# Performance work log

Measured on AMD Instinct MI355X. Metric: run time of the kernel, lower is better.

## Reference

```python
import jax, jax.numpy as jnp
import numpy as np

ALPHA = 0.4
MAX_STEPS = 10
GATE_WARMUP = 1.0

def _l2n(x):  # F.normalize(dim=-1), eps=1e-12
    return x / jnp.maximum(jnp.linalg.norm(x, axis=-1, keepdims=True), 1e-12)

def _ln(x, g, b):  # nn.LayerNorm, eps=1e-5
    m = jnp.mean(x, -1, keepdims=True)
    v = jnp.mean((x - m) ** 2, -1, keepdims=True)
    return (x - m) * jax.lax.rsqrt(v + 1e-5) * g + b

def _gelu(x):  # torch F.gelu default = exact erf
    return jax.nn.gelu(x, approximate=False)

def setup_inputs() -> dict:
    key = jax.random.key(0)
    ks = jax.random.split(key, 12)
    B, T, V, D, H = 4, 256, 50257, 768, 3072
    f32 = jnp.float32
    s = lambda k, shape, sc: jax.random.normal(k, shape, dtype=f32) * sc
    return {
        'token_ids': jax.random.randint(ks[0], (B, T), 0, V),
        'embedding': s(ks[1], (V, D), 0.02),      # nn.Embedding table
        'V0': s(ks[2], (D, H), 0.02), 'b0': jnp.zeros((H,), f32),  # hierarchy layer 0
        'V1': s(ks[3], (H, D), 0.02), 'b1': jnp.zeros((D,), f32),  # hierarchy layer 1
        'W1': s(ks[4], (D, D), 0.005), 'c1': jnp.zeros((D,), f32), # core_proj[0]
        'W2': s(ks[5], (D, D), 0.005), 'c2': jnp.zeros((D,), f32), # core_proj[2]
        'Wg': s(ks[6], (2 * D, D), 0.005), 'bg': jnp.zeros((D,), f32),  # gate_proj
        'Wt': s(ks[7], (D, D), 0.01),              # temporal_proj (no bias)
        'gamma': jnp.ones((D,), f32), 'beta': jnp.zeros((D,), f32),    # out_norm
        'Wl': s(ks[8], (D, V), 0.02),              # lm_head (no bias)
        'R_weight': s(ks[9], (D, D), 0.01),        # buffer (orthogonal-ish, small)
    }

def reference(token_ids, embedding, V0, b0, V1, b1, W1, c1, W2, c2, Wg, bg, Wt, gamma, beta, Wl, R_weight):
    B = token_ids.shape[0]
    D = embedding.shape[1]

    def step(carry, idx):
        h_prev, x2 = carry  # h_prev: [B,D] recurrent state; x2: settled hierarchy state [B,D]
        emb = _l2n(embedding[idx])                       # [B,D]
        h_prev_d = jax.lax.stop_gradient(h_prev)         # .detach()
        temporal_raw = h_prev_d @ R_weight               # [B,D]
        ctx = emb + ALPHA * temporal_raw
        # hierarchy.infer_and_learn under no_grad: iterative relaxation toward the
        # feedforward settled state over max_steps iterations.
        ctx_d = jax.lax.stop_gradient(ctx)
        target = _gelu(_gelu(ctx_d @ V0 + b0) @ V1 + b1)
        x2 = jax.lax.fori_loop(0, MAX_STEPS, lambda i, x: 0.5 * x + 0.5 * target, x2)
        x2 = jax.lax.stop_gradient(x2)
        core_settled = _l2n(x2)
        # differentiable shadow path through V0/b0/V1/b1
        core_shadow = _l2n(_gelu(_gelu(ctx @ V0 + b0) @ V1 + b1))
        core_blended = 0.5 * core_shadow + 0.5 * core_settled
        core_feat = _gelu(core_blended @ W1 + c1) @ W2 + c2      # core_proj MLP
        temporal_feat = temporal_raw @ Wt
        gate = jax.nn.sigmoid(jnp.concatenate([emb, core_feat], axis=-1) @ Wg + bg)
        g = gate * GATE_WARMUP
        h_t = g * (core_feat + ALPHA * temporal_feat) + (1.0 - g) * emb
        h_t = _ln(h_t, gamma, beta)
        logits = h_t @ Wl                                # [B,V]
        return (jax.lax.stop_gradient(h_t), x2), logits

    init = (jnp.zeros((B, D), embedding.dtype), jnp.zeros((B, D), embedding.dtype))
    _, logits = jax.lax.scan(step, init, token_ids.T)    # [T,B,V]
    return jnp.transpose(logits, (1, 0, 2))              # [B,T,V]
```

## Files before the change

### kernel.cpp

```cpp
#include <hip/hip_runtime.h>


typedef __attribute__((ext_vector_type(8))) short short8;
typedef __attribute__((ext_vector_type(4))) float f32x4;
typedef unsigned long long u64;

__device__ __forceinline__ unsigned short f2b(float f){
  unsigned int u = __builtin_bit_cast(unsigned int, f);
  u += 0x7fffu + ((u >> 16) & 1u);
  return (unsigned short)(u >> 16);
}
__device__ __forceinline__ float b2f(unsigned short v){
  return __builtin_bit_cast(float, ((unsigned int)v) << 16);
}
__device__ __forceinline__ float geluf(float x){
  return 0.5f * x * (1.0f + erff(x * 0.70710678118654752440f));
}
__device__ __forceinline__ float wsum(float v){
  #pragma unroll
  for (int o = 32; o; o >>= 1) v += __shfl_xor(v, o, 64);
  return v;
}
__device__ __forceinline__ u64 pk3t(float a, float b, float c, unsigned tag){
  return (u64)f2b(a) | ((u64)f2b(b) << 16) | ((u64)f2b(c) << 32) | ((u64)(tag & 0xffffu) << 48);
}
__device__ __forceinline__ void st64(u64* p, u64 v){
  __hip_atomic_store(p, v, __ATOMIC_RELAXED, __HIP_MEMORY_SCOPE_AGENT);
}
__device__ __forceinline__ void stflag(int* p, int v){
  __hip_atomic_store(p, v, __ATOMIC_RELAXED, __HIP_MEMORY_SCOPE_AGENT);
}
__device__ __forceinline__ int ldflag(const int* p){
  return __hip_atomic_load(p, __ATOMIC_RELAXED, __HIP_MEMORY_SCOPE_AGENT);
}
__device__ __forceinline__ void vm0(){ asm volatile("s_waitcnt vmcnt(0)" ::: "memory"); }

#define FA1  0
#define FTG  256
#define FU   512
#define FPRE 768
#define F2A1  1024
#define F2TG  1088
#define F2U   1152
#define F2PRE 1216

__global__ __launch_bounds__(256) void transpose_f2b(
    const float* __restrict__ src, unsigned short* __restrict__ dst,
    int N, int rowoff)
{
  __shared__ unsigned short tile[32][33];
  const int nb = blockIdx.x * 32, kb = blockIdx.y * 32;
  const int tx = threadIdx.x & 31, ty = threadIdx.x >> 5;
  #pragma unroll
  for (int i = 0; i < 4; ++i) {
    int k = kb + ty + 8*i, n = nb + tx;
    unsigned short v = 0;
    if (n < N) v = f2b(src[(size_t)(rowoff + k)*N + n]);
    tile[ty + 8*i][tx] = v;
  }
  __syncthreads();
  #pragma unroll
  for (int i = 0; i < 4; ++i) {
    int n = nb + ty + 8*i;
    if (n < N) dst[(size_t)n*768 + kb + tx] = tile[tx][ty + 8*i];
  }
}

__global__ __launch_bounds__(256) void embed_kernel(
    const int* __restrict__ tok, const float* __restrict__ emb,
    float* __restrict__ emb_all)
{
  const int row = blockIdx.x, tid = threadIdx.x;
  const int id = tok[row];
  const float* e = emb + (size_t)id * 768;
  float v0 = e[tid], v1 = e[tid+256], v2 = e[tid+512];
  float ssq = wsum(v0*v0 + v1*v1 + v2*v2);
  __shared__ float red[4];
  if ((tid & 63) == 0) red[tid >> 6] = ssq;
  __syncthreads();
  float inv = 1.0f / fmaxf(sqrtf(red[0]+red[1]+red[2]+red[3]), 1e-12f);
  float* o = emb_all + (size_t)row * 768;
  o[tid] = v0*inv; o[tid+256] = v1*inv; o[tid+512] = v2*inv;
}

__global__ void gbias_kernel(const float* __restrict__ c2,
                             const float* __restrict__ Wg,
                             float* __restrict__ gbias)
{
  int c = blockIdx.x * 256 + threadIdx.x;
  if (c >= 768) return;
  float s = 0.f;
  for (int k = 0; k < 768; ++k) s += c2[k] * Wg[(size_t)(768 + k)*768 + c];
  gbias[c] = s;
}

template<int BMODE>
__global__ __launch_bounds__(256) void gemm_kernel(
    const float* __restrict__ A, const void* __restrict__ Bp,
    float* __restrict__ C, const float* __restrict__ bias,
    int M, int N, int q, int r)
{
  const int x = blockIdx.x;
  const int s = blockIdx.y;
  const int mtiles = M >> 6;
  const int cnt_x = q + (x < r ? 1 : 0);
  if (s >= cnt_x * mtiles) return;
  const int off_x = x*q + (x < r ? x : r);
  const int nt = off_x + s / mtiles;
  const int mt = s % mtiles;
  const int m0 = mt << 6, n0 = nt << 6;
  const int w = threadIdx.x >> 6, l = threadIdx.x & 63;
  const int lrow = l & 15, lk8 = (l >> 4) << 3;
  const int arow = m0 + w*16 + lrow;
  f32x4 acc[4] = {f32x4{0,0,0,0}, f32x4{0,0,0,0}, f32x4{0,0,0,0}, f32x4{0,0,0,0}};
  const unsigned short* BT = (const unsigned short*)Bp;
  const float* Bf = (const float*)Bp;

  for (int kk = 0; kk < 768; kk += 32) {
    const float4* ap = (const float4*)(A + (size_t)arow*768 + kk + lk8);
    float4 a0 = ap[0], a1 = ap[1];
    short8 af;
    af[0]=(short)f2b(a0.x); af[1]=(short)f2b(a0.y); af[2]=(short)f2b(a0.z); af[3]=(short)f2b(a0.w);
    af[4]=(short)f2b(a1.x); af[5]=(short)f2b(a1.y); af[6]=(short)f2b(a1.z); af[7]=(short)f2b(a1.w);
    #pragma unroll
    for (int ss = 0; ss < 4; ++ss) {
      const int col = n0 + ss*16 + lrow;
      short8 bf;
      if (BMODE == 0) {
        if (col < N) {
          uint4 raw = *(const uint4*)(BT + (size_t)col*768 + kk + lk8);
          bf = __builtin_bit_cast(short8, raw);
        } else {
          bf = short8{0,0,0,0,0,0,0,0};
        }
      } else {
        #pragma unroll
        for (int j = 0; j < 8; ++j) {
          float v = (col < N) ? Bf[(size_t)(kk + lk8 + j)*N + col] : 0.f;
          bf[j] = (short)f2b(v);
        }
      }
      acc[ss] = __builtin_amdgcn_mfma_f32_16x16x32_bf16(af, bf, acc[ss], 0, 0, 0);
    }
  }
  const int rbase = m0 + w*16 + ((l >> 4) << 2);
  #pragma unroll
  for (int ss = 0; ss < 4; ++ss) {
    const int col = n0 + ss*16 + lrow;
    if (col < N) {
      const float badd = bias ? bias[col] : 0.f;
      #pragma unroll
      for (int rr = 0; rr < 4; ++rr)
        C[(size_t)(rbase + rr)*N + col] = acc[ss][rr] + badd;
    }
  }
}

__global__ __launch_bounds__(256) void recur_kernel(
    const float* __restrict__ RV0, const float* __restrict__ RWt,
    const float* __restrict__ W1,  const float* __restrict__ W2,
    const float* __restrict__ W2G, const float* __restrict__ V1,
    const float* __restrict__ embV0, const float* __restrict__ embWg,
    const float* __restrict__ gbias, const float* __restrict__ emb_all,
    const float* __restrict__ b1, const float* __restrict__ c1,
    const float* __restrict__ c2, const float* __restrict__ gam,
    const float* __restrict__ bet, float* __restrict__ h_all,
    u64* __restrict__ a1_if, u64* __restrict__ tg_if,
    u64* __restrict__ u_if,  u64* __restrict__ pre_if,
    int* __restrict__ flg)
{
  __shared__ float sRV0[12*768];
  __shared__ float sV1[3*3072];
  __shared__ float sW1[3*768];
  __shared__ float sW2[3*768];
  __shared__ float sW2G[3*768];
  __shared__ float sRWt[3*768];
  __shared__ float sX[4*768];
  __shared__ float sX2[4*768];
  __shared__ unsigned short sA1[4*3072];
  __shared__ float sRed[240];
  __shared__ float sTf[16];

  const int g = blockIdx.x, tid = threadIdx.x;
  const int wv = tid >> 6, lane = tid & 63;
  const bool isAgg = (g < 16);

  for (int i = tid; i < 12*768; i += 256) {
    int k = i / 12, c = i - k*12;
    sRV0[c*768 + k] = RV0[(size_t)k*3072 + g*12 + c];
  }
  for (int i = tid; i < 3*3072; i += 256) {
    int k = i / 3, c = i - k*3;
    sV1[c*3072 + k] = V1[(size_t)k*768 + g*3 + c];
  }
  for (int i = tid; i < 3*768; i += 256) {
    int k = i / 3, c = i - k*3;
    const int gc = g*3 + c;
    sW1[c*768 + k]  = W1[(size_t)k*768 + gc];
    sW2[c*768 + k]  = W2[(size_t)k*768 + gc];
    sW2G[c*768 + k] = W2G[(size_t)k*768 + gc];
    sRWt[c*768 + k] = RWt[(size_t)k*768 + gc];
  }
  for (int i = tid; i < 4*768; i += 256) sX2[i] = 0.f;
  __syncthreads();

  for (int t = 0; t <= 256; ++t) {
    if (t == 0) {
      for (int i = tid; i < 4*768; i += 256) sX[i] = 0.f;
    } else {
      if (isAgg) {
        if (tid < 16)
          while (ldflag(flg + FPRE + g*16 + tid) < t) __builtin_amdgcn_s_sleep(2);
        __syncthreads();
        if (tid == 0) stflag(flg + F2PRE + g, t);
      }
      if (tid < 16)
        while (ldflag(flg + F2PRE + tid) < t) __builtin_amdgcn_s_sleep(4);
      __syncthreads();
      const u64* pm = pre_if + (size_t)(t-1)*1024 + lane*16 + wv;
      u64 w4[4];
      #pragma unroll
      for (int qq = 0; qq < 4; ++qq) w4[qq] = pm[qq*4];
      float pre[12];
      #pragma unroll
      for (int qq = 0; qq < 4; ++qq) {
        pre[qq*3+0] = b2f((unsigned short)(w4[qq]));
        pre[qq*3+1] = b2f((unsigned short)(w4[qq] >> 16));
        pre[qq*3+2] = b2f((unsigned short)(w4[qq] >> 32));
      }
      float s1 = 0.f;
      #pragma unroll
      for (int i = 0; i < 12; ++i) s1 += pre[i];
      s1 = wsum(s1);
      const float mean = s1 * (1.0f/768.0f);
      float s2 = 0.f;
      #pragma unroll
      for (int i = 0; i < 12; ++i) { const float d = pre[i] - mean; s2 += d*d; }
      s2 = wsum(s2);
      const float rstd = 1.0f / sqrtf(s2*(1.0f/768.0f) + 1e-5f);
      const int k0 = lane*12;
      float hv[12];
      #pragma unroll
      for (int i = 0; i < 12; ++i) {
        hv[i] = (pre[i] - mean)*rstd*gam[k0+i] + bet[k0+i];
        sX[wv*768 + k0 + i] = hv[i];
      }
      if (g == 0) {
        float* hp = h_all + (size_t)(wv*256 + t - 1)*768 + k0;
        #pragma unroll
        for (int i = 0; i < 12; ++i) hp[i] = hv[i];
      }
    }
    __syncthreads();
    if (t == 256) break;
    const unsigned tagp = (unsigned)(t + 1);
    const int want = t + 1;

    {
      const int cg = tid >> 6, ks = tid & 63;
      float acc[4][4] = {};
      for (int i = 0; i < 12; ++i) {
        const int k = ks + 64*i;
        const float x0 = sX[k], x1 = sX[768+k], x2v = sX[1536+k], x3 = sX[2304+k];
        #pragma unroll
        for (int j = 0; j < 4; ++j) {
          float w;
          if (cg < 3) w = sRV0[(cg*4 + j)*768 + k];
          else        w = (j < 3) ? sRWt[j*768 + k] : 0.f;
          acc[j][0] += w*x0; acc[j][1] += w*x1; acc[j][2] += w*x2v; acc[j][3] += w*x3;
        }
      }
      #pragma unroll
      for (int j = 0; j < 4; ++j)
        #pragma unroll
        for (int bb = 0; bb < 4; ++bb) {
          const float v = wsum(acc[j][bb]);
          if (lane == 0) sRed[cg*16 + j*4 + bb] = v;
        }
      __syncthreads();
      if (tid < 16) {
        const int bb = tid & 3, w = tid >> 2;
        float v[3];
        #pragma unroll
        for (int s = 0; s < 3; ++s) {
          const int c = w*3 + s;
          const float raw = sRed[(c >> 2)*16 + (c & 3)*4 + bb];
          v[s] = geluf(embV0[(size_t)(bb*256 + t)*3072 + g*12 + c] + 0.4f*raw);
        }
        st64(a1_if + (size_t)t*4096 + bb*1024 + g*4 + w, pk3t(v[0], v[1], v[2], tagp));
      } else if (tid < 20) {
        const int bb = tid - 16;
        sTf[bb]     = sRed[48 + bb];
        sTf[4 + bb] = sRed[52 + bb];
        sTf[8 + bb] = sRed[56 + bb];
      }
      vm0();
      __syncthreads();
      if (tid == 0) stflag(flg + FA1 + g, want);
    }

    {
      if (isAgg) {
        if (tid < 16)
          while (ldflag(flg + FA1 + g*16 + tid) < want) __builtin_amdgcn_s_sleep(2);
        __syncthreads();
        if (tid == 0) stflag(flg + F2A1 + g, want);
      }
      if (tid < 16)
        while (ldflag(flg + F2A1 + tid) < want) __builtin_amdgcn_s_sleep(4);
      __syncthreads();
      const u64* basep = a1_if + (size_t)t*4096;
      u64 x[16];
      #pragma unroll
      for (int i = 0; i < 16; ++i) x[i] = basep[i*256 + tid];
      #pragma unroll
      for (int i = 0; i < 16; ++i) {
        const int widx = i*256 + tid;
        const int bb = widx >> 10, j = widx & 1023;
        sA1[bb*3072 + 3*j + 0] = (unsigned short)(x[i]);
        sA1[bb*3072 + 3*j + 1] = (unsigned short)(x[i] >> 16);
        sA1[bb*3072 + 3*j + 2] = (unsigned short)(x[i] >> 32);
      }
      __syncthreads();
      const int ks = lane, isub = wv;
      float acc[3][4] = {};
      for (int ip = 0; ip < 12; ++ip) {
        const int k = ks + 64*(isub + 4*ip);
        float xv[4];
        #pragma unroll
        for (int bb = 0; bb < 4; ++bb) xv[bb] = b2f(sA1[bb*3072 + k]);
        #pragma unroll
        for (int c = 0; c < 3; ++c) {
          const float w = sV1[c*3072 + k];
          acc[c][0] += w*xv[0]; acc[c][1] += w*xv[1]; acc[c][2] += w*xv[2]; acc[c][3] += w*xv[3];
        }
      }
      #pragma unroll
      for (int c = 0; c < 3; ++c)
        #pragma unroll
        for (int bb = 0; bb < 4; ++bb) {
          const float v = wsum(acc[c][bb]);
          if (lane == 0) sRed[isub*12 + c*4 + bb] = v;
        }
      __syncthreads();
      if (tid < 4) {
        const int bb = tid;
        float v[3];
        #pragma unroll
        for (int c = 0; c < 3; ++c) {
          float s = sRed[c*4+bb] + sRed[12 + c*4+bb] + sRed[24 + c*4+bb] + sRed[36 + c*4+bb];
          v[c] = geluf(s + b1[g*3 + c]);
        }
        st64(tg_if + (size_t)t*1024 + g*4 + bb, pk3t(v[0], v[1], v[2], tagp));
      }
      vm0();
      __syncthreads();
      if (tid == 0) stflag(flg + FTG + g, want);
    }

    {
      if (isAgg) {
        if (tid < 16)
          while (ldflag(flg + FTG + g*16 + tid) < want) __builtin_amdgcn_s_sleep(2);
        __syncthreads();
        if (tid == 0) stflag(flg + F2TG + g, want);
      }
      if (tid < 16)
        while (ldflag(flg + F2TG + tid) < want) __builtin_amdgcn_s_sleep(4);
      __syncthreads();
      const u64* pm = tg_if + (size_t)t*1024 + lane*16 + wv;
      u64 w4[4];
      #pragma unroll
      for (int qq = 0; qq < 4; ++qq) w4[qq] = pm[qq*4];
      float tv[12];
      #pragma unroll
      for (int qq = 0; qq < 4; ++qq) {
        tv[qq*3+0] = b2f((unsigned short)(w4[qq]));
        tv[qq*3+1] = b2f((unsigned short)(w4[qq] >> 16));
        tv[qq*3+2] = b2f((unsigned short)(w4[qq] >> 32));
      }
      const int xb = wv*768 + lane*12;
      float xv2[12];
      float ssqT = 0.f, ssqX = 0.f;
      #pragma unroll
      for (int i = 0; i < 12; ++i) {
        float xx = sX2[xb + i];
        const float tt = tv[i];
        #pragma unroll
        for (int rr = 0; rr < 10; ++rr) xx = 0.5f*xx + 0.5f*tt;
        sX2[xb + i] = xx; xv2[i] = xx;
        ssqT += tt*tt; ssqX += xx*xx;
      }
      ssqT = wsum(ssqT); ssqX = wsum(ssqX);
      const float invT = 1.0f / fmaxf(sqrtf(ssqT), 1e-12f);
      const float invX = 1.0f / fmaxf(sqrtf(ssqX), 1e-12f);
      #pragma unroll
      for (int i = 0; i < 12; ++i) sX[xb + i] = 0.5f*(tv[i]*invT + xv2[i]*invX);
      __syncthreads();
      const int ks = lane, isub = wv;
      float acc[3][4] = {};
      #pragma unroll
      for (int ip = 0; ip < 3; ++ip) {
        const int k = ks + 64*(isub + 4*ip);
        float xv[4];
        #pragma unroll
        for (int bb = 0; bb < 4; ++bb) xv[bb] = sX[bb*768 + k];
        #pragma unroll
        for (int c = 0; c < 3; ++c) {
          const float w = sW1[c*768 + k];
          acc[c][0] += w*xv[0]; acc[c][1] += w*xv[1]; acc[c][2] += w*xv[2]; acc[c][3] += w*xv[3];
        }
      }
      #pragma unroll
      for (int c = 0; c < 3; ++c)
        #pragma unroll
        for (int bb = 0; bb < 4; ++bb) {
          const float v = wsum(acc[c][bb]);
          if (lane == 0) sRed[isub*12 + c*4 + bb] = v;
        }
      __syncthreads();
      if (tid < 4) {
        const int bb = tid;
        float v[3];
        #pragma unroll
        for (int c = 0; c < 3; ++c) {
          float s = sRed[c*4+bb] + sRed[12 + c*4+bb] + sRed[24 + c*4+bb] + sRed[36 + c*4+bb];
          v[c] = geluf(s + c1[g*3 + c]);
        }
        st64(u_if + (size_t)t*1024 + g*4 + bb, pk3t(v[0], v[1], v[2], tagp));
      }
      vm0();
      __syncthreads();
      if (tid == 0) stflag(flg + FU + g, want);
    }

    {
      if (isAgg) {
        if (tid < 16)
          while (ldflag(flg + FU + g*16 + tid) < want) __builtin_amdgcn_s_sleep(2);
        __syncthreads();
        if (tid == 0) stflag(flg + F2U + g, want);
      }
      if (tid < 16)
        while (ldflag(flg + F2U + tid) < want) __builtin_amdgcn_s_sleep(4);
      __syncthreads();
      const u64* pm = u_if + (size_t)t*1024 + lane*16 + wv;
      u64 w4[4];
      #pragma unroll
      for (int qq = 0; qq < 4; ++qq) w4[qq] = pm[qq*4];
      const int xb = wv*768 + lane*12;
      #pragma unroll
      for (int qq = 0; qq < 4; ++qq) {
        sX[xb + qq*3 + 0] = b2f((unsigned short)(w4[qq]));
        sX[xb + qq*3 + 1] = b2f((unsigned short)(w4[qq] >> 16));
        sX[xb + qq*3 + 2] = b2f((unsigned short)(w4[qq] >> 32));
      }
      __syncthreads();
      const int ks = lane, isub = wv;
      float acc[6][4] = {};
      #pragma unroll
      for (int ip = 0; ip < 3; ++ip) {
        const int k = ks + 64*(isub + 4*ip);
        float xv[4];
        #pragma unroll
        for (int bb = 0; bb < 4; ++bb) xv[bb] = sX[bb*768 + k];
        #pragma unroll
        for (int c = 0; c < 6; ++c) {
          const float w = (c < 3) ? sW2[c*768 + k] : sW2G[(c-3)*768 + k];
          acc[c][0] += w*xv[0]; acc[c][1] += w*xv[1]; acc[c][2] += w*xv[2]; acc[c][3] += w*xv[3];
        }
      }
      #pragma unroll
      for (int c = 0; c < 6; ++c)
        #pragma unroll
        for (int bb = 0; bb < 4; ++bb) {
          const float v = wsum(acc[c][bb]);
          if (lane == 0) sRed[isub*24 + c*4 + bb] = v;
        }
      __syncthreads();
      if (tid < 4) {
        const int bb = tid;
        float pre3[3];
        #pragma unroll
        for (int c = 0; c < 3; ++c) {
          const int col = g*3 + c;
          float sc = sRed[c*4+bb] + sRed[24 + c*4+bb] + sRed[48 + c*4+bb] + sRed[72 + c*4+bb];
          const float cf = sc + c2[col];
          const int cc = c + 3;
          float sg = sRed[cc*4+bb] + sRed[24 + cc*4+bb] + sRed[48 + cc*4+bb] + sRed[72 + cc*4+bb];
          const float gv = sg + embWg[(size_t)(bb*256 + t)*768 + col] + gbias[col];
          const float gg = 1.0f / (1.0f + expf(-gv));
          const float em = emb_all[(size_t)(bb*256 + t)*768 + col];
          pre3[c] = gg*(cf + 0.4f*sTf[c*4 + bb]) + (1.0f - gg)*em;
        }
        st64(pre_if + (size_t)t*1024 + g*4 + bb, pk3t(pre3[0], pre3[1], pre3[2], tagp));
      }
      vm0();
      __syncthreads();
      if (tid == 0) stflag(flg + FPRE + g, want);
    }
  }
}

static void launch_gemm(const float* A, const void* B, float* C, const float* bias,
                        int M, int N, int bmode, hipStream_t st)
{
  const int ntiles = (N + 63) / 64;
  const int q = ntiles / 8, r = ntiles % 8;
  const int mtiles = M / 64;
  const int smax = (q + (r ? 1 : 0)) * mtiles;
  dim3 grid(8, smax);
  if (bmode == 0) gemm_kernel<0><<<grid, 256, 0, st>>>(A, B, C, bias, M, N, q, r);
  else            gemm_kernel<1><<<grid, 256, 0, st>>>(A, B, C, bias, M, N, q, r);
}

extern "C" void kernel_launch(void* const* d_in, const int* in_sizes, int n_in,
                              void* d_out, int out_size, void* d_ws, size_t ws_size,
                              hipStream_t stream)
{
  const int*   tok   = (const int*)d_in[0];
  const float* emb   = (const float*)d_in[1];
  const float* V0    = (const float*)d_in[2];
  const float* b0    = (const float*)d_in[3];
  const float* V1    = (const float*)d_in[4];
  const float* b1    = (const float*)d_in[5];
  const float* W1    = (const float*)d_in[6];
  const float* c1    = (const float*)d_in[7];
  const float* W2    = (const float*)d_in[8];
  const float* c2    = (const float*)d_in[9];
  const float* Wg    = (const float*)d_in[10];
  const float* bg    = (const float*)d_in[11];
  const float* Wt    = (const float*)d_in[12];
  const float* gamma = (const float*)d_in[13];
  const float* beta  = (const float*)d_in[14];
  const float* Wl    = (const float*)d_in[15];
  const float* Rw    = (const float*)d_in[16];

  float* outf = (float*)d_out;
  float* emb_all = outf + 0;
  float* RV0     = outf + 786432;
  float* RWt     = outf + 3145728;
  float* W2G     = outf + 3735552;
  float* embV0   = outf + 4325376;
  float* embWg   = outf + 7471104;
  float* gbias   = outf + 8257536;
  unsigned short* V0T  = (unsigned short*)(outf + 8258560);
  unsigned short* WtT  = (unsigned short*)(outf + 9438208);
  unsigned short* WgTT = (unsigned short*)(outf + 9733120);
  unsigned short* WgBT = (unsigned short*)(outf + 10028032);
  u64* a1_if  = (u64*)(outf + 10322944);
  u64* tg_if  = (u64*)(outf + 12428288);
  u64* u_if   = (u64*)(outf + 12954624);
  u64* pre_if = (u64*)(outf + 13480960);
  int* flg    = (int*)(outf + 14007296);

  float* h_all = (float*)d_ws;
  unsigned short* WlT = (unsigned short*)((char*)d_ws + 786432*4);
  const bool bigws = ws_size >= (size_t)(786432*4) + (size_t)38597376*2 + 256;

  hipMemsetAsync(flg, 0, 2048 * sizeof(int), stream);

  transpose_f2b<<<dim3(96, 24),   256, 0, stream>>>(V0, V0T, 3072, 0);
  transpose_f2b<<<dim3(24, 24),   256, 0, stream>>>(Wt, WtT, 768, 0);
  transpose_f2b<<<dim3(24, 24),   256, 0, stream>>>(Wg, WgTT, 768, 0);
  transpose_f2b<<<dim3(24, 24),   256, 0, stream>>>(Wg, WgBT, 768, 768);
  if (bigws)
    transpose_f2b<<<dim3(1572, 24), 256, 0, stream>>>(Wl, WlT, 50257, 0);

  embed_kernel<<<1024, 256, 0, stream>>>(tok, emb, emb_all);
  gbias_kernel<<<3, 256, 0, stream>>>(c2, Wg, gbias);

  launch_gemm(Rw,      V0T,  RV0,   nullptr, 768,  3072, 0, stream);
  launch_gemm(Rw,      WtT,  RWt,   nullptr, 768,  768,  0, stream);
  launch_gemm(W2,      WgBT, W2G,   nullptr, 768,  768,  0, stream);
  launch_gemm(emb_all, V0T,  embV0, b0,      1024, 3072, 0, stream);
  launch_gemm(emb_all, WgTT, embWg, bg,      1024, 768,  0, stream);

  recur_kernel<<<256, 256, 0, stream>>>(
      RV0, RWt, W1, W2, W2G, V1, embV0, embWg, gbias, emb_all,
      b1, c1, c2, gamma, beta, h_all,
      a1_if, tg_if, u_if, pre_if, flg);

  if (bigws) launch_gemm(h_all, WlT, outf, nullptr, 1024, 50257, 0, stream);
  else       launch_gemm(h_all, Wl,  outf, nullptr, 1024, 50257, 1, stream);
}
```

Baseline: 10.39 ms.

## Pad sync flags to separate cache lines and prefetch per-step inputs into LDS

Spaces each synchronisation flag 16 ints apart so block flags no longer share cache lines, which should cut false-sharing traffic during spin-waits. It also prefetches per-step embV0, embWg and emb slices into shared memory at the top of each step, and caches biases and LayerNorm gamma/beta in registers or LDS so they are not reloaded from global memory in the serial critical path. Spin sleep intervals for non-aggregator waits are lengthened. It adds an unused emb_all float4 load and a larger flag memset, and the flag region now spans 17408 ints, which must fit in the output-buffer space reserved for it.

```diff
diff --git a/kernel.cpp b/kernel.cpp
--- a/kernel.cpp
+++ b/kernel.cpp
@@ -35,14 +35,8 @@
 }
 __device__ __forceinline__ void vm0(){ asm volatile("s_waitcnt vmcnt(0)" ::: "memory"); }
 
-#define FA1  0
-#define FTG  256
-#define FU   512
-#define FPRE 768
-#define F2A1  1024
-#define F2TG  1088
-#define F2U   1152
-#define F2PRE 1216
+#define F0(ph,g) (((ph)*256 + (g))*16)
+#define F1(ph,a) (16384 + ((ph)*16 + (a))*16)
 
 __global__ __launch_bounds__(256) void transpose_f2b(
     const float* __restrict__ src, unsigned short* __restrict__ dst,
@@ -180,6 +174,10 @@
   __shared__ unsigned short sA1[4*3072];
   __shared__ float sRed[240];
   __shared__ float sTf[16];
+  __shared__ float sCst[12];
+  __shared__ float sEV0[48];
+  __shared__ float sEWg[12];
+  __shared__ float sEmb[12];
 
   const int g = blockIdx.x, tid = threadIdx.x;
   const int wv = tid >> 6, lane = tid & 63;
@@ -202,20 +200,47 @@
     sRWt[c*768 + k] = RWt[(size_t)k*768 + gc];
   }
   for (int i = tid; i < 4*768; i += 256) sX2[i] = 0.f;
+  if (tid < 3)       sCst[tid]     = b1[g*3 + tid];
+  else if (tid < 6)  sCst[tid]     = c1[g*3 + tid - 3];
+  else if (tid < 9)  sCst[tid]     = c2[g*3 + tid - 6];
+  else if (tid < 12) sCst[tid]     = gbias[g*3 + tid - 9];
+  const int k0 = lane*12;
+  float gamv[12], betv[12];
+  #pragma unroll
+  for (int i = 0; i < 12; ++i) { gamv[i] = gam[k0+i]; betv[i] = bet[k0+i]; }
   __syncthreads();
 
   for (int t = 0; t <= 256; ++t) {
+    if (t < 256) {
+      if (tid >= 64 && tid < 112) {
+        const int j = tid - 64, bb = j & 3, c = j >> 2;
+        sEV0[c*4 + bb] = embV0[(size_t)(bb*256 + t)*3072 + g*12 + c];
+      } else if (tid >= 128 && tid < 140) {
+        const int j = tid - 128, bb = j & 3, c = j >> 2;
+        sEWg[c*4 + bb] = embWg[(size_t)(bb*256 + t)*768 + g*3 + c];
+      } else if (tid >= 140 && tid < 152) {
+        const int j = tid - 140, bb = j & 3, c = j >> 2;
+        sEmb[c*4 + bb] = emb_all[(size_t)(bb*256 + t)*768 + g*3 + c];
+      }
+    }
+
     if (t == 0) {
       for (int i = tid; i < 4*768; i += 256) sX[i] = 0.f;
     } else {
+      float4 e0, e1, e2;
+      {
+        const float4* q4 = (const float4*)(emb_all + (size_t)(wv*256 + t - 1)*768 + lane*12);
+        e0 = q4[0]; e1 = q4[1]; e2 = q4[2];
+      }
+      (void)e0; (void)e1; (void)e2;
       if (isAgg) {
         if (tid < 16)
-          while (ldflag(flg + FPRE + g*16 + tid) < t) __builtin_amdgcn_s_sleep(2);
+          while (ldflag(flg + F0(3, g*16 + tid)) < t) __builtin_amdgcn_s_sleep(2);
         __syncthreads();
-        if (tid == 0) stflag(flg + F2PRE + g, t);
+        if (tid == 0) stflag(flg + F1(3, g), t);
       }
       if (tid < 16)
-        while (ldflag(flg + F2PRE + tid) < t) __builtin_amdgcn_s_sleep(4);
+        while (ldflag(flg + F1(3, tid)) < t) __builtin_amdgcn_s_sleep(8);
       __syncthreads();
       const u64* pm = pre_if + (size_t)(t-1)*1024 + lane*16 + wv;
       u64 w4[4];
@@ -238,11 +263,10 @@
       for (int i = 0; i < 12; ++i) { const float d = pre[i] - mean; s2 += d*d; }
       s2 = wsum(s2);
       const float rstd = 1.0f / sqrtf(s2*(1.0f/768.0f) + 1e-5f);
-      const int k0 = lane*12;
       float hv[12];
       #pragma unroll
       for (int i = 0; i < 12; ++i) {
-        hv[i] = (pre[i] - mean)*rstd*gam[k0+i] + bet[k0+i];
+        hv[i] = (pre[i] - mean)*rstd*gamv[i] + betv[i];
         sX[wv*768 + k0 + i] = hv[i];
       }
       if (g == 0) {
@@ -285,7 +309,7 @@
         for (int s = 0; s < 3; ++s) {
           const int c = w*3 + s;
           const float raw = sRed[(c >> 2)*16 + (c & 3)*4 + bb];
-          v[s] = geluf(embV0[(size_t)(bb*256 + t)*3072 + g*12 + c] + 0.4f*raw);
+          v[s] = geluf(sEV0[c*4 + bb] + 0.4f*raw);
         }
         st64(a1_if + (size_t)t*4096 + bb*1024 + g*4 + w, pk3t(v[0], v[1], v[2], tagp));
       } else if (tid < 20) {
@@ -296,18 +320,18 @@
       }
       vm0();
       __syncthreads();
-      if (tid == 0) stflag(flg + FA1 + g, want);
+      if (tid == 0) stflag(flg + F0(0, g), want);
     }
 
     {
       if (isAgg) {
         if (tid < 16)
-          while (ldflag(flg + FA1 + g*16 + tid) < want) __builtin_amdgcn_s_sleep(2);
+          while (ldflag(flg + F0(0, g*16 + tid)) < want) __builtin_amdgcn_s_sleep(2);
         __syncthreads();
-        if (tid == 0) stflag(flg + F2A1 + g, want);
+        if (tid == 0) stflag(flg + F1(0, g), want);
       }
       if (tid < 16)
-        while (ldflag(flg + F2A1 + tid) < want) __builtin_amdgcn_s_sleep(4);
+        while (ldflag(flg + F1(0, tid)) < want) __builtin_amdgcn_s_sleep(8);
       __syncthreads();
       const u64* basep = a1_if + (size_t)t*4096;
       u64 x[16];
@@ -349,24 +373,24 @@
         #pragma unroll
         for (int c = 0; c < 3; ++c) {
           float s = sRed[c*4+bb] + sRed[12 + c*4+bb] + sRed[24 + c*4+bb] + sRed[36 + c*4+bb];
-          v[c] = geluf(s + b1[g*3 + c]);
+          v[c] = geluf(s + sCst[c]);
         }
         st64(tg_if + (size_t)t*1024 + g*4 + bb, pk3t(v[0], v[1], v[2], tagp));
       }
       vm0();
       __syncthreads();
-      if (tid == 0) stflag(flg + FTG + g, want);
+      if (tid == 0) stflag(flg + F0(1, g), want);
     }
 
     {
       if (isAgg) {
         if (tid < 16)
-          while (ldflag(flg + FTG + g*16 + tid) < want) __builtin_amdgcn_s_sleep(2);
+          while (ldflag(flg + F0(1, g*16 + tid)) < want) __builtin_amdgcn_s_sleep(2);
         __syncthreads();
-        if (tid == 0) stflag(flg + F2TG + g, want);
+        if (tid == 0) stflag(flg + F1(1, g), want);
       }
       if (tid < 16)
-        while (ldflag(flg + F2TG + tid) < want) __builtin_amdgcn_s_sleep(4);
+        while (ldflag(flg + F1(1, tid)) < want) __builtin_amdgcn_s_sleep(8);
       __syncthreads();
       const u64* pm = tg_if + (size_t)t*1024 + lane*16 + wv;
       u64 w4[4];
@@ -425,24 +449,24 @@
         #pragma unroll
         for (int c = 0; c < 3; ++c) {
           float s = sRed[c*4+bb] + sRed[12 + c*4+bb] + sRed[24 + c*4+bb] + sRed[36 + c*4+bb];
-          v[c] = geluf(s + c1[g*3 + c]);
+          v[c] = geluf(s + sCst[3 + c]);
         }
         st64(u_if + (size_t)t*1024 + g*4 + bb, pk3t(v[0], v[1], v[2], tagp));
       }
       vm0();
       __syncthreads();
-      if (tid == 0) stflag(flg + FU + g, want);
+      if (tid == 0) stflag(flg + F0(2, g), want);
     }
 
     {
       if (isAgg) {
         if (tid < 16)
-          while (ldflag(flg + FU + g*16 + tid) < want) __builtin_amdgcn_s_sleep(2);
+          while (ldflag(flg + F0(2, g*16 + tid)) < want) __builtin_amdgcn_s_sleep(2);
         __syncthreads();
-        if (tid == 0) stflag(flg + F2U + g, want);
+        if (tid == 0) stflag(flg + F1(2, g), want);
       }
       if (tid < 16)
-        while (ldflag(flg + F2U + tid) < want) __builtin_amdgcn_s_sleep(4);
+        while (ldflag(flg + F1(2, tid)) < want) __builtin_amdgcn_s_sleep(8);
       __syncthreads();
       const u64* pm = u_if + (size_t)t*1024 + lane*16 + wv;
       u64 w4[4];
@@ -483,21 +507,20 @@
         float pre3[3];
         #pragma unroll
         for (int c = 0; c < 3; ++c) {
-          const int col = g*3 + c;
           float sc = sRed[c*4+bb] + sRed[24 + c*4+bb] + sRed[48 + c*4+bb] + sRed[72 + c*4+bb];
-          const float cf = sc + c2[col];
+          const float cf = sc + sCst[6 + c];
           const int cc = c + 3;
           float sg = sRed[cc*4+bb] + sRed[24 + cc*4+bb] + sRed[48 + cc*4+bb] + sRed[72 + cc*4+bb];
-          const float gv = sg + embWg[(size_t)(bb*256 + t)*768 + col] + gbias[col];
+          const float gv = sg + sEWg[c*4 + bb] + sCst[9 + c];
           const float gg = 1.0f / (1.0f + expf(-gv));
-          const float em = emb_all[(size_t)(bb*256 + t)*768 + col];
+          const float em = sEmb[c*4 + bb];
           pre3[c] = gg*(cf + 0.4f*sTf[c*4 + bb]) + (1.0f - gg)*em;
         }
         st64(pre_if + (size_t)t*1024 + g*4 + bb, pk3t(pre3[0], pre3[1], pre3[2], tagp));
       }
       vm0();
       __syncthreads();
-      if (tid == 0) stflag(flg + FPRE + g, want);
+      if (tid == 0) stflag(flg + F0(3, g), want);
     }
   }
 }
@@ -558,7 +581,7 @@
   unsigned short* WlT = (unsigned short*)((char*)d_ws + 786432*4);
   const bool bigws = ws_size >= (size_t)(786432*4) + (size_t)38597376*2 + 256;
 
-  hipMemsetAsync(flg, 0, 2048 * sizeof(int), stream);
+  hipMemsetAsync(flg, 0, 17408 * sizeof(int), stream);
 
   transpose_f2b<<<dim3(96, 24),   256, 0, stream>>>(V0, V0T, 3072, 0);
   transpose_f2b<<<dim3(24, 24),   256, 0, stream>>>(Wt, WtT, 768, 0);
```

Result: faster. 8.768 ms (-15.6%).
